# Kernel tuning notes

Hardware: AMD Instinct MI355X
Metric: run time of the kernel (lower is better)

## Reference

```python
import jax, jax.numpy as jnp
import numpy as np

TEMPERATURE = 1.0
NEG_INF = -1e30  # finite stand-in for -inf: safe for log_softmax and its vjp


def setup_inputs() -> dict:
    key = jax.random.key(0)
    k1, k2 = jax.random.split(key)
    B, M, D = 4096, 3, 256
    tokens = jax.random.normal(k1, (B, M, D), dtype=jnp.float32)
    labels = jax.random.randint(k2, (B,), 0, 32, dtype=jnp.int32)
    return {"tokens": tokens, "labels": labels}


def reference(tokens, labels):
    # tokens: [B, M, D]; labels: [B]
    B, M, D = tokens.shape
    # Pairwise per-modality similarities: sim[i, k, m] = <tokens[i,m], tokens[k,m]>
    sim = jnp.einsum('imd,kmd->ikm', tokens, tokens) / TEMPERATURE
    self_mask = jnp.eye(B, dtype=bool)
    # Original excludes sample i itself from the candidate set; masking with a
    # huge negative logit makes it contribute 0 to the softmax partition.
    sim = jnp.where(self_mask[:, :, None], NEG_INF, sim)
    logp = jax.nn.log_softmax(sim, axis=1)  # softmax over the B-1 other samples

    # Positive pairs: same label, excluding self.
    pos = (labels[:, None] == labels[None, :]) & ~self_mask  # [B, B]
    pos_count = pos.sum(axis=1)                               # [B]
    valid = pos_count > 0                                     # sum(same_label) > 1

    # Mean log-prob over positives, per (sample, modality).
    pos_logp = jnp.einsum('ikm,ik->im', logp, pos.astype(logp.dtype))  # [B, M]
    denom = jnp.maximum(pos_count, 1).astype(logp.dtype)[:, None]
    per = jnp.where(valid[:, None], pos_logp / denom, 0.0)             # [B, M]

    num = valid.sum() * M
    return -per.sum() / num.astype(per.dtype)
```

## Files before the change

kernel.cpp:

```cpp
#include <hip/hip_runtime.h>

#define B_N 4096
#define M_N 3
#define D_N 256
#define LOG2E 1.44269504088896340736f
#define LN2   0.69314718055994530942f
#define C_OFF   64.0f
#define T_CLAMP 112.0f

typedef __bf16 bf16x8 __attribute__((ext_vector_type(8)));
typedef float  f32x4  __attribute__((ext_vector_type(4)));

__device__ __forceinline__ unsigned short f2bf(float f) {
    unsigned int u = __float_as_uint(f);
    u += 0x7FFFu + ((u >> 16) & 1u);
    return (unsigned short)(u >> 16);
}
__device__ __forceinline__ float bf2f(unsigned short h) {
    return __uint_as_float(((unsigned int)h) << 16);
}

__global__ void cvt_kernel(const float* __restrict__ in, unsigned short* __restrict__ out,
                           float* __restrict__ norm2) {
    int idx = blockIdx.x * blockDim.x + threadIdx.x;
    float4 v = reinterpret_cast<const float4*>(in)[idx];
    int i   = idx / 192;
    int rem = idx - i * 192;
    int m   = rem >> 6;
    int d4  = rem & 63;
    ushort4 o;
    o.x = f2bf(v.x); o.y = f2bf(v.y); o.z = f2bf(v.z); o.w = f2bf(v.w);
    reinterpret_cast<ushort4*>(out)[((size_t)m * B_N + i) * 64 + d4] = o;
    float nx = bf2f(o.x), ny = bf2f(o.y), nz = bf2f(o.z), nw = bf2f(o.w);
    float s = nx * nx + ny * ny + nz * nz + nw * nw;
#pragma unroll
    for (int msk = 1; msk < 64; msk <<= 1) s += __shfl_xor(s, msk);
    if ((threadIdx.x & 63) == 0) norm2[m * B_N + i] = s;
}

__global__ __launch_bounds__(256, 3) void main_kernel(
    const unsigned short* __restrict__ tokb, const int* __restrict__ labels,
    float2* __restrict__ partials) {
    int raw = blockIdx.x;
    int bid = (raw & 7) * 198 + (raw >> 3);
    int m    = bid / 528;
    int beta = bid - m * 528;
    int b = 0;
    while ((b + 1) * (b + 2) / 2 <= beta) ++b;
    int a = beta - (b * (b + 1)) / 2;
    bool offd = (a != b);
    int cb = b * 128;

    int tid  = threadIdx.x;
    int wave = tid >> 6, lane = tid & 63;
    int lr = lane & 15, lk = lane >> 4;
    const unsigned short* tm = tokb + (size_t)m * (B_N * D_N);

    __shared__ __align__(16) char ldsB[2][8192];
    __shared__ int labl[128];
    __shared__ float colbuf[4][8][16][2];
    if (tid < 128) labl[tid] = labels[cb + tid];

    int r0 = a * 128 + wave * 32;
    bf16x8 afrag[2][8];
#pragma unroll
    for (int rt = 0; rt < 2; ++rt) {
        const unsigned short* rp = tm + (size_t)(r0 + rt * 16 + lr) * D_N + lk * 8;
#pragma unroll
        for (int kf = 0; kf < 8; ++kf)
            afrag[rt][kf] = *reinterpret_cast<const bf16x8*>(rp + kf * 32);
    }
    int labr[2][4];
#pragma unroll
    for (int rt = 0; rt < 2; ++rt)
#pragma unroll
        for (int j = 0; j < 4; ++j)
            labr[rt][j] = labels[r0 + rt * 16 + lk * 4 + j];

    float S[2][4] = {{0.f, 0.f, 0.f, 0.f}, {0.f, 0.f, 0.f, 0.f}};
    float P[2][4] = {{0.f, 0.f, 0.f, 0.f}, {0.f, 0.f, 0.f, 0.f}};

    int lc  = tid >> 5;
    int w   = tid & 31;
    int sch = w ^ (lc & 7);
    const unsigned short* sbase = tm + (size_t)(cb + lc) * D_N + sch * 8;

    {
        bf16x8 t0 = *reinterpret_cast<const bf16x8*>(sbase);
        bf16x8 t1 = *reinterpret_cast<const bf16x8*>(sbase + 8 * D_N);
        *reinterpret_cast<bf16x8*>(&ldsB[0][tid * 16])        = t0;
        *reinterpret_cast<bf16x8*>(&ldsB[0][4096 + tid * 16]) = t1;
    }

    for (int kb = 0; kb < 8; ++kb) {
        int cur = kb & 1;
        __syncthreads();

        int nkb = (kb + 1) & 7;
        const unsigned short* np = sbase + (size_t)nkb * (16 * D_N);
        bf16x8 nt0 = *reinterpret_cast<const bf16x8*>(np);
        bf16x8 nt1 = *reinterpret_cast<const bf16x8*>(np + 8 * D_N);

        const char* bp = ldsB[cur];
        int swz = (lr & 7) << 4;
        bf16x8 bfrag[8];
#pragma unroll
        for (int kf = 0; kf < 8; ++kf)
            bfrag[kf] = *reinterpret_cast<const bf16x8*>(
                bp + lr * 512 + (((kf * 4 + lk) << 4) ^ swz));
        int labc = labl[kb * 16 + lr];

        f32x4 acc0 = {0.f, 0.f, 0.f, 0.f};
        f32x4 acc1 = {0.f, 0.f, 0.f, 0.f};
#pragma unroll
        for (int kf = 0; kf < 8; ++kf) {
            acc0 = __builtin_amdgcn_mfma_f32_16x16x32_bf16(afrag[0][kf], bfrag[kf], acc0, 0, 0, 0);
            acc1 = __builtin_amdgcn_mfma_f32_16x16x32_bf16(afrag[1][kf], bfrag[kf], acc1, 0, 0, 0);
        }

        float cs = 0.f, cp = 0.f;
        int cg0 = cb + kb * 16;
        if ((cg0 < r0 + 32) && (cg0 + 16 > r0)) {
            int colg = cg0 + lr;
#pragma unroll
            for (int rt = 0; rt < 2; ++rt) {
                f32x4 aa = rt ? acc1 : acc0;
#pragma unroll
                for (int j = 0; j < 4; ++j) {
                    float s2 = aa[j];
                    float t = fminf(fmaf(s2, LOG2E, -C_OFF), T_CLAMP);
                    float e = __builtin_amdgcn_exp2f(t);
                    int row = r0 + rt * 16 + lk * 4 + j;
                    e = (colg == row) ? 0.f : e;
                    bool mt = (labc == labr[rt][j]);
                    S[rt][j] += e;  P[rt][j] += mt ? s2 : 0.f;
                    cs += e;        cp += mt ? s2 : 0.f;
                }
            }
        } else {
#pragma unroll
            for (int rt = 0; rt < 2; ++rt) {
                f32x4 aa = rt ? acc1 : acc0;
#pragma unroll
                for (int j = 0; j < 4; ++j) {
                    float s2 = aa[j];
                    float t = fminf(fmaf(s2, LOG2E, -C_OFF), T_CLAMP);
                    float e = __builtin_amdgcn_exp2f(t);
                    bool mt = (labc == labr[rt][j]);
                    S[rt][j] += e;  P[rt][j] += mt ? s2 : 0.f;
                    cs += e;        cp += mt ? s2 : 0.f;
                }
            }
        }

        cs += __shfl_xor(cs, 16); cs += __shfl_xor(cs, 32);
        cp += __shfl_xor(cp, 16); cp += __shfl_xor(cp, 32);
        if (lk == 0) { colbuf[wave][kb][lr][0] = cs; colbuf[wave][kb][lr][1] = cp; }

        char* dst = (char*)ldsB[cur ^ 1];
        *reinterpret_cast<bf16x8*>(dst + tid * 16)        = nt0;
        *reinterpret_cast<bf16x8*>(dst + 4096 + tid * 16) = nt1;
    }

    __syncthreads();

#pragma unroll
    for (int rt = 0; rt < 2; ++rt)
#pragma unroll
        for (int j = 0; j < 4; ++j) {
            float sv = S[rt][j], pv = P[rt][j];
#pragma unroll
            for (int msk = 1; msk < 16; msk <<= 1) {
                sv += __shfl_xor(sv, msk);
                pv += __shfl_xor(pv, msk);
            }
            if (lr == 0) {
                int row = r0 + rt * 16 + lk * 4 + j;
                float2 q; q.x = sv; q.y = pv;
                partials[(size_t)(b * 3 + m) * B_N + row] = q;
            }
        }

    if (offd && tid < 128) {
        int kb = tid >> 4, cr = tid & 15;
        float sv = colbuf[0][kb][cr][0] + colbuf[1][kb][cr][0]
                 + colbuf[2][kb][cr][0] + colbuf[3][kb][cr][0];
        float pv = colbuf[0][kb][cr][1] + colbuf[1][kb][cr][1]
                 + colbuf[2][kb][cr][1] + colbuf[3][kb][cr][1];
        int col = cb + tid;
        float2 q; q.x = sv; q.y = pv;
        partials[(size_t)(a * 3 + m) * B_N + col] = q;
    }
}

__global__ void reduce_kernel(const float2* __restrict__ partials,
                              const float* __restrict__ norm2,
                              const int* __restrict__ labels,
                              float* __restrict__ blockpart,
                              int* __restrict__ nvout) {
    __shared__ int h[32];
    int tid = threadIdx.x;
    if (tid < 32) h[tid] = 0;
    __syncthreads();
    for (int i = tid; i < B_N; i += 256) atomicAdd(&h[labels[i]], 1);
    __syncthreads();
    if (blockIdx.x == 0 && tid == 0) {
        int nv = 0;
#pragma unroll
        for (int c = 0; c < 32; ++c) nv += (h[c] >= 2) ? h[c] : 0;
        nvout[0] = nv;
    }
    int gid = blockIdx.x * 256 + tid;
    int m = gid >> 12, i = gid & 4095;
    float S = 0.f, P = 0.f;
#pragma unroll
    for (int s = 0; s < 32; ++s) {
        float2 q = partials[(size_t)(s * 3 + m) * B_N + i];
        S += q.x; P += q.y;
    }
    P -= norm2[gid];
    int pc = h[labels[i]] - 1;
    float contrib = (pc > 0)
        ? (__builtin_amdgcn_logf(S) + C_OFF) * LN2 - P / (float)pc
        : 0.f;
#pragma unroll
    for (int off = 32; off >= 1; off >>= 1) contrib += __shfl_down(contrib, off);
    __shared__ float w4[4];
    if ((tid & 63) == 0) w4[tid >> 6] = contrib;
    __syncthreads();
    if (tid == 0) blockpart[blockIdx.x] = w4[0] + w4[1] + w4[2] + w4[3];
}

__global__ void final_kernel(const float* __restrict__ blockpart, const int* __restrict__ nv,
                             float* __restrict__ out) {
    int lane = threadIdx.x;
    float s = (lane < 48) ? blockpart[lane] : 0.f;
#pragma unroll
    for (int off = 32; off >= 1; off >>= 1) s += __shfl_down(s, off);
    if (lane == 0) out[0] = s / (float)(nv[0] * M_N);
}

extern "C" void kernel_launch(void* const* d_in, const int* in_sizes, int n_in,
                              void* d_out, int out_size, void* d_ws, size_t ws_size,
                              hipStream_t stream) {
    const float* tokens = (const float*)d_in[0];
    const int*   labels = (const int*)d_in[1];
    float* out = (float*)d_out;

    char* ws = (char*)d_ws;
    int*    nv        = (int*)(ws + 128);
    float*  blockpart = (float*)(ws + 256);
    float*  norm2     = (float*)(ws + 1024);
    float2* partials  = (float2*)(ws + 65536);
    unsigned short* tokb = (unsigned short*)(ws + 3407872);

    cvt_kernel<<<3072, 256, 0, stream>>>(tokens, tokb, norm2);
    main_kernel<<<1584, 256, 0, stream>>>(tokb, labels, partials);
    reduce_kernel<<<48, 256, 0, stream>>>(partials, norm2, labels, blockpart, nv);
    final_kernel<<<1, 64, 0, stream>>>(blockpart, nv, out);
}
```

Measured before the change: 51.11 us.

## Fuse fp32-to-bf16 conversion and norm computation into main kernel

Removes the separate conversion kernel and its bf16 workspace. The main kernel now reads fp32 tokens directly, converts them to bf16 in registers for both A fragments and LDS B tiles, and diagonal blocks compute the squared norms. This saves one launch and the write and re-read of the bf16 copy. In exchange, each block loads twice the bytes per tile with a strided layout, and the conversion is repeated across the many blocks that reuse the same rows.

```diff
diff --git a/kernel.cpp b/kernel.cpp
--- a/kernel.cpp
+++ b/kernel.cpp
@@ -11,36 +11,22 @@
 typedef __bf16 bf16x8 __attribute__((ext_vector_type(8)));
 typedef float  f32x4  __attribute__((ext_vector_type(4)));
 
-__device__ __forceinline__ unsigned short f2bf(float f) {
-    unsigned int u = __float_as_uint(f);
-    u += 0x7FFFu + ((u >> 16) & 1u);
-    return (unsigned short)(u >> 16);
-}
 __device__ __forceinline__ float bf2f(unsigned short h) {
     return __uint_as_float(((unsigned int)h) << 16);
 }
 
-__global__ void cvt_kernel(const float* __restrict__ in, unsigned short* __restrict__ out,
-                           float* __restrict__ norm2) {
-    int idx = blockIdx.x * blockDim.x + threadIdx.x;
-    float4 v = reinterpret_cast<const float4*>(in)[idx];
-    int i   = idx / 192;
-    int rem = idx - i * 192;
-    int m   = rem >> 6;
-    int d4  = rem & 63;
-    ushort4 o;
-    o.x = f2bf(v.x); o.y = f2bf(v.y); o.z = f2bf(v.z); o.w = f2bf(v.w);
-    reinterpret_cast<ushort4*>(out)[((size_t)m * B_N + i) * 64 + d4] = o;
-    float nx = bf2f(o.x), ny = bf2f(o.y), nz = bf2f(o.z), nw = bf2f(o.w);
-    float s = nx * nx + ny * ny + nz * nz + nw * nw;
-#pragma unroll
-    for (int msk = 1; msk < 64; msk <<= 1) s += __shfl_xor(s, msk);
-    if ((threadIdx.x & 63) == 0) norm2[m * B_N + i] = s;
+__device__ __forceinline__ bf16x8 cvt8(const float* __restrict__ p) {
+    float4 u0 = *reinterpret_cast<const float4*>(p);
+    float4 u1 = *reinterpret_cast<const float4*>(p + 4);
+    bf16x8 r;
+    r[0] = (__bf16)u0.x; r[1] = (__bf16)u0.y; r[2] = (__bf16)u0.z; r[3] = (__bf16)u0.w;
+    r[4] = (__bf16)u1.x; r[5] = (__bf16)u1.y; r[6] = (__bf16)u1.z; r[7] = (__bf16)u1.w;
+    return r;
 }
 
 __global__ __launch_bounds__(256, 3) void main_kernel(
-    const unsigned short* __restrict__ tokb, const int* __restrict__ labels,
-    float2* __restrict__ partials) {
+    const float* __restrict__ tokens, const int* __restrict__ labels,
+    float2* __restrict__ partials, float* __restrict__ norm2) {
     int raw = blockIdx.x;
     int bid = (raw & 7) * 198 + (raw >> 3);
     int m    = bid / 528;
@@ -54,7 +40,6 @@
     int tid  = threadIdx.x;
     int wave = tid >> 6, lane = tid & 63;
     int lr = lane & 15, lk = lane >> 4;
-    const unsigned short* tm = tokb + (size_t)m * (B_N * D_N);
 
     __shared__ __align__(16) char ldsB[2][8192];
     __shared__ int labl[128];
@@ -65,10 +50,10 @@
     bf16x8 afrag[2][8];
 #pragma unroll
     for (int rt = 0; rt < 2; ++rt) {
-        const unsigned short* rp = tm + (size_t)(r0 + rt * 16 + lr) * D_N + lk * 8;
+        const float* rp = tokens + ((size_t)(r0 + rt * 16 + lr) * 3 + m) * 256 + lk * 8;
 #pragma unroll
         for (int kf = 0; kf < 8; ++kf)
-            afrag[rt][kf] = *reinterpret_cast<const bf16x8*>(rp + kf * 32);
+            afrag[rt][kf] = cvt8(rp + kf * 32);
     }
     int labr[2][4];
 #pragma unroll
@@ -76,6 +61,23 @@
 #pragma unroll
         for (int j = 0; j < 4; ++j)
             labr[rt][j] = labels[r0 + rt * 16 + lk * 4 + j];
+
+    if (!offd) {
+#pragma unroll
+        for (int rt = 0; rt < 2; ++rt) {
+            float nrm = 0.f;
+#pragma unroll
+            for (int kf = 0; kf < 8; ++kf)
+#pragma unroll
+                for (int e = 0; e < 8; ++e) {
+                    float x = (float)afrag[rt][kf][e];
+                    nrm = fmaf(x, x, nrm);
+                }
+            nrm += __shfl_xor(nrm, 16);
+            nrm += __shfl_xor(nrm, 32);
+            if (lk == 0) norm2[m * B_N + r0 + rt * 16 + lr] = nrm;
+        }
+    }
 
     float S[2][4] = {{0.f, 0.f, 0.f, 0.f}, {0.f, 0.f, 0.f, 0.f}};
     float P[2][4] = {{0.f, 0.f, 0.f, 0.f}, {0.f, 0.f, 0.f, 0.f}};
@@ -83,11 +85,12 @@
     int lc  = tid >> 5;
     int w   = tid & 31;
     int sch = w ^ (lc & 7);
-    const unsigned short* sbase = tm + (size_t)(cb + lc) * D_N + sch * 8;
+    const float* sb0 = tokens + ((size_t)(cb + lc) * 3 + m) * 256 + sch * 8;
+    const float* sb1 = sb0 + 8 * 768;
 
     {
-        bf16x8 t0 = *reinterpret_cast<const bf16x8*>(sbase);
-        bf16x8 t1 = *reinterpret_cast<const bf16x8*>(sbase + 8 * D_N);
+        bf16x8 t0 = cvt8(sb0);
+        bf16x8 t1 = cvt8(sb1);
         *reinterpret_cast<bf16x8*>(&ldsB[0][tid * 16])        = t0;
         *reinterpret_cast<bf16x8*>(&ldsB[0][4096 + tid * 16]) = t1;
     }
@@ -97,9 +100,8 @@
         __syncthreads();
 
         int nkb = (kb + 1) & 7;
-        const unsigned short* np = sbase + (size_t)nkb * (16 * D_N);
-        bf16x8 nt0 = *reinterpret_cast<const bf16x8*>(np);
-        bf16x8 nt1 = *reinterpret_cast<const bf16x8*>(np + 8 * D_N);
+        bf16x8 nt0 = cvt8(sb0 + (size_t)nkb * 12288);
+        bf16x8 nt1 = cvt8(sb1 + (size_t)nkb * 12288);
 
         const char* bp = ldsB[cur];
         int swz = (lr & 7) << 4;
@@ -252,10 +254,8 @@
     float*  blockpart = (float*)(ws + 256);
     float*  norm2     = (float*)(ws + 1024);
     float2* partials  = (float2*)(ws + 65536);
-    unsigned short* tokb = (unsigned short*)(ws + 3407872);
-
-    cvt_kernel<<<3072, 256, 0, stream>>>(tokens, tokb, norm2);
-    main_kernel<<<1584, 256, 0, stream>>>(tokb, labels, partials);
+
+    main_kernel<<<1584, 256, 0, stream>>>(tokens, labels, partials, norm2);
     reduce_kernel<<<48, 256, 0, stream>>>(partials, norm2, labels, blockpart, nv);
     final_kernel<<<1, 64, 0, stream>>>(blockpart, nv, out);
 }
```

New measurement: 63.85 us. 1.25x slower.
